# Kernel tuning notes

Hardware: AMD Instinct MI355X
Metric: run time of the kernel (lower is better)

The kernel has to match this reference:

```python
import jax, jax.numpy as jnp
import numpy as np
from jax import lax

T, L, K = 1024, 32, 128
BEG = 0  # index of '[BEG]' in the label dict


def setup_inputs() -> dict:
    key = jax.random.key(0)
    kx, kw, kl = jax.random.split(key, 3)
    X = jax.random.normal(kx, (T, L, L, K), dtype=jnp.float32)
    w = jax.random.normal(kw, (K,), dtype=jnp.float32)  # nn.Parameter, init N(0,1)
    label = jax.random.randint(kl, (T,), 0, L, dtype=jnp.int32)
    return {"X": X, "w": w, "label": label}


def reference(X, w, label):
    """CRF negative log-likelihood (forward algorithm over log-potential matrices)."""
    # Ms[t, i, j] = log-potential of transition i->j at step t  (X @ w)
    Ms = jnp.einsum('tijk,k->tij', X, w)  # [T, L, L]

    # forward recurrence: alpha_t[j] = logsumexp_i(alpha_{t-1}[i] + Ms[t, i, j])
    alpha0 = Ms[0, BEG, :]  # [L]

    def step(alpha, M):
        new = jax.nn.logsumexp(alpha[:, None] + M, axis=0)
        return new, None

    alpha_last, _ = lax.scan(step, alpha0, Ms[1:])
    logZ = jax.nn.logsumexp(alpha_last)

    # gold-path score: sum_t Ms[t, prev_label_t, label_t], prev_0 = BEG
    prev = jnp.concatenate([jnp.array([BEG], dtype=label.dtype), label[:-1]])
    t_idx = jnp.arange(Ms.shape[0])
    path_score = jnp.sum(Ms[t_idx, prev, label])

    return -path_score + logZ
```

## Files before the change

### kernel.cpp

```cpp
#include <hip/hip_runtime.h>

#define TT 1024
#define LL 32
#define CHUNK 4
#define NBLK (TT / CHUNK)

#define ALPHA0_OFF 0
#define PATH_OFF   32
#define P0_OFF     288
#define Q1_OFF     (P0_OFF + 256 * 1024)
#define Q2_OFF     (Q1_OFF + 32 * 1024)

__device__ __forceinline__ float lse_cell(const float A[LL][LL + 1],
                                          const float B[LL][LL + 1],
                                          int i, int j) {
  float s[LL];
  #pragma unroll
  for (int k = 0; k < LL; k++) s[k] = A[i][k] + B[k][j];
  float t[16];
  #pragma unroll
  for (int k = 0; k < 16; k++) t[k] = fmaxf(s[k], s[k + 16]);
  #pragma unroll
  for (int st = 8; st >= 1; st >>= 1) {
    #pragma unroll
    for (int k = 0; k < st; k++) t[k] = fmaxf(t[k], t[k + st]);
  }
  const float mx = t[0];
  float a0 = 0.f, a1 = 0.f, a2 = 0.f, a3 = 0.f;
  #pragma unroll
  for (int k = 0; k < LL; k += 4) {
    a0 += __expf(s[k]     - mx);
    a1 += __expf(s[k + 1] - mx);
    a2 += __expf(s[k + 2] - mx);
    a3 += __expf(s[k + 3] - mx);
  }
  return mx + __logf((a0 + a1) + (a2 + a3));
}

__global__ __launch_bounds__(1024, 1) void crf_stageA(
    const float4* __restrict__ X4, const float* __restrict__ w,
    const int* __restrict__ label, float* __restrict__ ws) {
  __shared__ float Ms[CHUNK][LL][LL + 1];
  __shared__ float Pb[2][LL][LL + 1];
  const int blk = blockIdx.x, tid = threadIdx.x;
  const int l5 = tid & 31;
  const int half = (tid >> 5) & 1;
  const int wid = tid >> 6;
  const int cellbase = wid * 2 + half;
  const float4 w4 = reinterpret_cast<const float4*>(w)[l5];
  const int t0 = blk * CHUNK;

  #pragma unroll
  for (int m = 0; m < CHUNK; m++) {
    #pragma unroll 8
    for (int it = 0; it < LL; it++) {
      const int cell = it * LL + cellbase;
      float4 xv = X4[(size_t)(t0 + m) * 1024u * 32u + (size_t)cell * 32u + l5];
      float v = fmaf(xv.x, w4.x, fmaf(xv.y, w4.y, fmaf(xv.z, w4.z, xv.w * w4.w)));
      v += __shfl_xor(v, 16, 32);
      v += __shfl_xor(v,  8, 32);
      v += __shfl_xor(v,  4, 32);
      v += __shfl_xor(v,  2, 32);
      v += __shfl_xor(v,  1, 32);
      if (l5 == 0) Ms[m][it][cellbase] = v;
    }
  }
  __syncthreads();

  if (tid == 0) {
    float ps = 0.f;
    for (int m = 0; m < CHUNK; m++) {
      const int t = t0 + m;
      const int lab = label[t];
      const int pv = (t == 0) ? 0 : label[t - 1];
      ps += Ms[m][pv][lab];
    }
    ws[PATH_OFF + blk] = ps;
  }
  if (blk == 0 && tid < LL) ws[ALPHA0_OFF + tid] = Ms[0][0][tid];

  const int i = tid >> 5, j = tid & 31;
  const int first = (blk == 0) ? 1 : 0;
  Pb[0][i][j] = lse_cell(Ms[first], Ms[first + 1], i, j);
  int cur = 0;
  for (int m = first + 2; m < CHUNK; m++) {
    __syncthreads();
    float r = lse_cell(Pb[cur], Ms[m], i, j);
    Pb[cur ^ 1][i][j] = r;
    cur ^= 1;
  }
  ws[P0_OFF + blk * 1024 + tid] = Pb[cur][i][j];
}

__global__ __launch_bounds__(1024, 1) void crf_comb8(
    const float* __restrict__ src, float* __restrict__ dst) {
  __shared__ float S[8][LL][LL + 1];
  __shared__ float PQ[4][LL][LL + 1];
  const int blk = blockIdx.x, tid = threadIdx.x;
  const int i = tid >> 5, j = tid & 31;
  #pragma unroll
  for (int m = 0; m < 8; m++)
    S[m][i][j] = src[((size_t)blk * 8 + m) * 1024 + tid];
  __syncthreads();
  #pragma unroll
  for (int q = 0; q < 4; q++)
    PQ[q][i][j] = lse_cell(S[2 * q], S[2 * q + 1], i, j);
  __syncthreads();
  S[0][i][j] = lse_cell(PQ[0], PQ[1], i, j);
  S[1][i][j] = lse_cell(PQ[2], PQ[3], i, j);
  __syncthreads();
  dst[(size_t)blk * 1024 + tid] = lse_cell(S[0], S[1], i, j);
}

__global__ __launch_bounds__(1024, 1) void crf_final4(
    const float* __restrict__ ws, float* __restrict__ out) {
  __shared__ float S[4][LL][LL + 1];
  __shared__ float PQ[2][LL][LL + 1];
  __shared__ float redm[16], reds[16], redp[16];
  const int tid = threadIdx.x, i = tid >> 5, j = tid & 31;
  #pragma unroll
  for (int m = 0; m < 4; m++) S[m][i][j] = ws[Q2_OFF + m * 1024 + tid];
  __syncthreads();
  PQ[0][i][j] = lse_cell(S[0], S[1], i, j);
  PQ[1][i][j] = lse_cell(S[2], S[3], i, j);
  __syncthreads();
  const float a = lse_cell(PQ[0], PQ[1], i, j);
  const float v = ws[ALPHA0_OFF + i] + a;

  float mx = v;
  #pragma unroll
  for (int o = 32; o >= 1; o >>= 1) mx = fmaxf(mx, __shfl_xor(mx, o));
  const int wv = tid >> 6, lane = tid & 63;
  if (lane == 0) redm[wv] = mx;
  __syncthreads();
  float mb = redm[0];
  #pragma unroll
  for (int q = 1; q < 16; q++) mb = fmaxf(mb, redm[q]);
  float e = __expf(v - mb);
  float p = (tid < 256) ? ws[PATH_OFF + tid] : 0.f;
  #pragma unroll
  for (int o = 32; o >= 1; o >>= 1) {
    e += __shfl_xor(e, o);
    p += __shfl_xor(p, o);
  }
  if (lane == 0) { reds[wv] = e; redp[wv] = p; }
  __syncthreads();
  if (tid == 0) {
    float s = 0.f, ps = 0.f;
    for (int q = 0; q < 16; q++) { s += reds[q]; ps += redp[q]; }
    out[0] = -ps + (mb + __logf(s));
  }
}

extern "C" void kernel_launch(void* const* d_in, const int* in_sizes, int n_in,
                              void* d_out, int out_size, void* d_ws, size_t ws_size,
                              hipStream_t stream) {
  const float4* X4 = (const float4*)d_in[0];
  const float* w = (const float*)d_in[1];
  const int* label = (const int*)d_in[2];
  float* out = (float*)d_out;
  float* ws = (float*)d_ws;

  crf_stageA<<<NBLK, 1024, 0, stream>>>(X4, w, label, ws);
  crf_comb8<<<32, 1024, 0, stream>>>(ws + P0_OFF, ws + Q1_OFF);
  crf_comb8<<<4, 1024, 0, stream>>>(ws + Q1_OFF, ws + Q2_OFF);
  crf_final4<<<1, 1024, 0, stream>>>(ws, out);
}
```

Before: 156.4 us.

## Halve stage-A chunk to two steps with 512-thread blocks and rebalance reduction tree

Stage A now handles two timesteps per block using 512 threads, so the grid doubles to 512 blocks and up to four blocks can share a CU. The projection loop is flattened over all cells of the chunk, and each thread computes two output cells of the single 32x32 log-sum-exp product. This removes the serial chain of three dependent combines per block. The later tree levels are resized to match (64 and 8 blocks, then a final kernel that combines 8 matrices), which adds one combine level in the final single-block kernel.

```diff
diff --git a/kernel.cpp b/kernel.cpp
--- a/kernel.cpp
+++ b/kernel.cpp
@@ -2,14 +2,14 @@
 
 #define TT 1024
 #define LL 32
-#define CHUNK 4
+#define CHUNK 2
 #define NBLK (TT / CHUNK)
 
 #define ALPHA0_OFF 0
 #define PATH_OFF   32
-#define P0_OFF     288
-#define Q1_OFF     (P0_OFF + 256 * 1024)
-#define Q2_OFF     (Q1_OFF + 32 * 1024)
+#define P0_OFF     544
+#define Q1_OFF     (P0_OFF + 512 * 1024)
+#define Q2_OFF     (Q1_OFF + 64 * 1024)
 
 __device__ __forceinline__ float lse_cell(const float A[LL][LL + 1],
                                           const float B[LL][LL + 1],
@@ -37,38 +37,37 @@
   return mx + __logf((a0 + a1) + (a2 + a3));
 }
 
-__global__ __launch_bounds__(1024, 1) void crf_stageA(
+__global__ __launch_bounds__(512, 4) void crf_stageA(
     const float4* __restrict__ X4, const float* __restrict__ w,
     const int* __restrict__ label, float* __restrict__ ws) {
   __shared__ float Ms[CHUNK][LL][LL + 1];
-  __shared__ float Pb[2][LL][LL + 1];
   const int blk = blockIdx.x, tid = threadIdx.x;
   const int l5 = tid & 31;
-  const int half = (tid >> 5) & 1;
-  const int wid = tid >> 6;
-  const int cellbase = wid * 2 + half;
+  const int grp = tid >> 5;
   const float4 w4 = reinterpret_cast<const float4*>(w)[l5];
+  const size_t base = (size_t)blk * (CHUNK * 1024) * 32;
   const int t0 = blk * CHUNK;
 
-  #pragma unroll
-  for (int m = 0; m < CHUNK; m++) {
-    #pragma unroll 8
-    for (int it = 0; it < LL; it++) {
-      const int cell = it * LL + cellbase;
-      float4 xv = X4[(size_t)(t0 + m) * 1024u * 32u + (size_t)cell * 32u + l5];
-      float v = fmaf(xv.x, w4.x, fmaf(xv.y, w4.y, fmaf(xv.z, w4.z, xv.w * w4.w)));
-      v += __shfl_xor(v, 16, 32);
-      v += __shfl_xor(v,  8, 32);
-      v += __shfl_xor(v,  4, 32);
-      v += __shfl_xor(v,  2, 32);
-      v += __shfl_xor(v,  1, 32);
-      if (l5 == 0) Ms[m][it][cellbase] = v;
+  #pragma unroll 4
+  for (int q = 0; q < 128; q++) {
+    const int cell = q * 16 + grp;
+    float4 xv = X4[base + (size_t)cell * 32 + l5];
+    float v = fmaf(xv.x, w4.x, fmaf(xv.y, w4.y, fmaf(xv.z, w4.z, xv.w * w4.w)));
+    v += __shfl_xor(v, 16, 32);
+    v += __shfl_xor(v,  8, 32);
+    v += __shfl_xor(v,  4, 32);
+    v += __shfl_xor(v,  2, 32);
+    v += __shfl_xor(v,  1, 32);
+    if (l5 == 0) {
+      const int m = cell >> 10, rem = cell & 1023;
+      Ms[m][rem >> 5][rem & 31] = v;
     }
   }
   __syncthreads();
 
   if (tid == 0) {
     float ps = 0.f;
+    #pragma unroll
     for (int m = 0; m < CHUNK; m++) {
       const int t = t0 + m;
       const int lab = label[t];
@@ -80,16 +79,16 @@
   if (blk == 0 && tid < LL) ws[ALPHA0_OFF + tid] = Ms[0][0][tid];
 
   const int i = tid >> 5, j = tid & 31;
-  const int first = (blk == 0) ? 1 : 0;
-  Pb[0][i][j] = lse_cell(Ms[first], Ms[first + 1], i, j);
-  int cur = 0;
-  for (int m = first + 2; m < CHUNK; m++) {
-    __syncthreads();
-    float r = lse_cell(Pb[cur], Ms[m], i, j);
-    Pb[cur ^ 1][i][j] = r;
-    cur ^= 1;
+  float r0, r1;
+  if (blk == 0) {
+    r0 = Ms[1][i][j];
+    r1 = Ms[1][i + 16][j];
+  } else {
+    r0 = lse_cell(Ms[0], Ms[1], i, j);
+    r1 = lse_cell(Ms[0], Ms[1], i + 16, j);
   }
-  ws[P0_OFF + blk * 1024 + tid] = Pb[cur][i][j];
+  ws[P0_OFF + (size_t)blk * 1024 + i * 32 + j] = r0;
+  ws[P0_OFF + (size_t)blk * 1024 + (i + 16) * 32 + j] = r1;
 }
 
 __global__ __launch_bounds__(1024, 1) void crf_comb8(
@@ -112,19 +111,23 @@
   dst[(size_t)blk * 1024 + tid] = lse_cell(S[0], S[1], i, j);
 }
 
-__global__ __launch_bounds__(1024, 1) void crf_final4(
+__global__ __launch_bounds__(1024, 1) void crf_final8(
     const float* __restrict__ ws, float* __restrict__ out) {
-  __shared__ float S[4][LL][LL + 1];
-  __shared__ float PQ[2][LL][LL + 1];
+  __shared__ float S[8][LL][LL + 1];
+  __shared__ float PQ[4][LL][LL + 1];
   __shared__ float redm[16], reds[16], redp[16];
   const int tid = threadIdx.x, i = tid >> 5, j = tid & 31;
   #pragma unroll
-  for (int m = 0; m < 4; m++) S[m][i][j] = ws[Q2_OFF + m * 1024 + tid];
+  for (int m = 0; m < 8; m++) S[m][i][j] = ws[Q2_OFF + m * 1024 + tid];
   __syncthreads();
-  PQ[0][i][j] = lse_cell(S[0], S[1], i, j);
-  PQ[1][i][j] = lse_cell(S[2], S[3], i, j);
+  #pragma unroll
+  for (int q = 0; q < 4; q++)
+    PQ[q][i][j] = lse_cell(S[2 * q], S[2 * q + 1], i, j);
   __syncthreads();
-  const float a = lse_cell(PQ[0], PQ[1], i, j);
+  S[0][i][j] = lse_cell(PQ[0], PQ[1], i, j);
+  S[1][i][j] = lse_cell(PQ[2], PQ[3], i, j);
+  __syncthreads();
+  const float a = lse_cell(S[0], S[1], i, j);
   const float v = ws[ALPHA0_OFF + i] + a;
 
   float mx = v;
@@ -137,7 +140,7 @@
   #pragma unroll
   for (int q = 1; q < 16; q++) mb = fmaxf(mb, redm[q]);
   float e = __expf(v - mb);
-  float p = (tid < 256) ? ws[PATH_OFF + tid] : 0.f;
+  float p = (tid < 512) ? ws[PATH_OFF + tid] : 0.f;
   #pragma unroll
   for (int o = 32; o >= 1; o >>= 1) {
     e += __shfl_xor(e, o);
@@ -161,8 +164,8 @@
   float* out = (float*)d_out;
   float* ws = (float*)d_ws;
 
-  crf_stageA<<<NBLK, 1024, 0, stream>>>(X4, w, label, ws);
-  crf_comb8<<<32, 1024, 0, stream>>>(ws + P0_OFF, ws + Q1_OFF);
-  crf_comb8<<<4, 1024, 0, stream>>>(ws + Q1_OFF, ws + Q2_OFF);
-  crf_final4<<<1, 1024, 0, stream>>>(ws, out);
+  crf_stageA<<<NBLK, 512, 0, stream>>>(X4, w, label, ws);
+  crf_comb8<<<64, 1024, 0, stream>>>(ws + P0_OFF, ws + Q1_OFF);
+  crf_comb8<<<8, 1024, 0, stream>>>(ws + Q1_OFF, ws + Q2_OFF);
+  crf_final8<<<1, 1024, 0, stream>>>(ws, out);
 }
```

Result: slower. 161.2 us (+3.1%).
